# Kernel tuning notes

Measured on AMD Instinct MI355X. Metric: run time of the kernel, lower is better.

Reference implementation:

```python
import jax, jax.numpy as jnp
import numpy as np

N = 32768   # 'a' nodes
K = 8       # incoming edges per node (regular graph)
K2 = K // 2
E = N * K   # edges, stored as reverse pairs (2i, 2i+1)
D = 300     # hid_dim
H = 4       # attention heads
DEPTH = 3


def _build_graph():
    i = np.arange(N)
    src = np.empty(E, np.int64)
    mail = np.empty((N, K), np.int64)
    for d in range(1, K2 + 1):
        base = 2 * (i * K2 + (d - 1))
        src[base] = i                 # edge i -> (i+d)%N
        src[base + 1] = (i + d) % N   # reverse edge (i+d)%N -> i
        # incoming edges of node v: ((v-d)->v) and ((v+d)->v)
        mail[:, 2 * (d - 1)] = 2 * (((i - d) % N) * K2 + (d - 1))
        mail[:, 2 * (d - 1) + 1] = 2 * (i * K2 + (d - 1)) + 1
    return src, mail


def setup_inputs() -> dict:
    key = jax.random.key(0)
    ks = jax.random.split(key, 12)
    s = 1.0 / np.sqrt(D)
    src, mail = _build_graph()
    return {
        'f': jax.random.normal(ks[0], (N, D), jnp.float32),
        'x': jax.random.normal(ks[1], (E, D), jnp.float32),
        'mail_idx': jnp.asarray(mail),
        'src_idx': jnp.asarray(src),
        'Wq': jax.random.normal(ks[2], (D, D), jnp.float32) * s,
        'bq': jnp.zeros((D,), jnp.float32),
        'Wk': jax.random.normal(ks[3], (D, D), jnp.float32) * s,
        'bk': jnp.zeros((D,), jnp.float32),
        'Wv': jax.random.normal(ks[4], (D, D), jnp.float32) * s,
        'bv': jnp.zeros((D,), jnp.float32),
        'Wo': jax.random.normal(ks[5], (D, D), jnp.float32) * s,
        'bo': jnp.zeros((D,), jnp.float32),
        'Wmp': jax.random.normal(ks[6], (DEPTH - 1, D, D), jnp.float32) * s,
        'bmp': jnp.zeros((DEPTH - 1, D), jnp.float32),
        'Wlast': jax.random.normal(ks[7], (3 * D, D), jnp.float32) * s,
        'blast': jnp.zeros((D,), jnp.float32),
    }


def _mha(q_in, k_in, v_in, Wq, bq, Wk, bk, Wv, bv, Wo, bo):
    # q_in: [N,1,D], k_in/v_in: [N,K,D]  (per-node neighborhood attention)
    dk = D // H
    q = (q_in @ Wq + bq).reshape(N, 1, H, dk).transpose(0, 2, 1, 3)
    k = (k_in @ Wk + bk).reshape(N, -1, H, dk).transpose(0, 2, 1, 3)
    v = (v_in @ Wv + bv).reshape(N, -1, H, dk).transpose(0, 2, 1, 3)
    scores = jnp.einsum('nhqd,nhkd->nhqk', q, k) / jnp.sqrt(jnp.float32(dk))
    p = jax.nn.softmax(scores, axis=-1)
    o = jnp.einsum('nhqk,nhkd->nhqd', p, v).transpose(0, 2, 1, 3).reshape(N, 1, D)
    return o @ Wo + bo


def reference(f, x, mail_idx, src_idx, Wq, bq, Wk, bk, Wv, bv, Wo, bo,
              Wmp, bmp, Wlast, blast):
    rev = jnp.arange(E) ^ 1  # reverse_edge: swap within consecutive pairs
    f_h = f              # init_node: f_h = f.clone()
    h = x                # init_edge: h = x.clone()
    for i in range(DEPTH - 1):
        mail = h[mail_idx]                    # copy_e mailbox [N,K,D]
        feat = f_h[:, None, :]                # [N,1,D]
        # add_attn: attn(feat, mail, mail + feat)
        f_h = _mha(feat, mail, mail + feat,
                   Wq, bq, Wk, bk, Wv, bv, Wo, bo)[:, 0, :]
        rev_h = h[rev]                        # paired reverse-edge feature
        m = f_h[src_idx] - rev_h              # del_reverse_message
        h = jax.nn.relu(x + m @ Wmp[i] + bmp[i])  # update_edge
    # final node update: Linear(cat([sum(mailbox h), f_h, f]))
    mail_sum = jnp.sum(h[mail_idx], axis=1)   # [N,D]
    f_final = jnp.concatenate([mail_sum, f_h, f], axis=1) @ Wlast + blast
    return f_final
```

## Files before the change

kernel.cpp:

```cpp
#include <hip/hip_runtime.h>

typedef unsigned short u16;
typedef unsigned int u32;
typedef __bf16 bf16x8 __attribute__((ext_vector_type(8)));
typedef float f32x4 __attribute__((ext_vector_type(4)));

#define N_NODES 32768
#define E_EDGES 262144
#define BQ_U16 26240
#define S75 0.11547005383792515f

__device__ __forceinline__ float b2f(u16 u) {
    union { u32 u; float f; } x; x.u = ((u32)u) << 16; return x.f;
}
__device__ __forceinline__ u16 f2b(float f) {
    union { float f; u32 u; } x; x.f = f;
    u32 r = x.u + 0x7FFF + ((x.u >> 16) & 1);
    return (u16)(r >> 16);
}
__device__ __forceinline__ u32 bsub2(u32 a, u32 b) {
    float lo = b2f((u16)(a & 0xFFFF)) - b2f((u16)(b & 0xFFFF));
    float hi = b2f((u16)(a >> 16))    - b2f((u16)(b >> 16));
    return (u32)f2b(lo) | ((u32)f2b(hi) << 16);
}

#define GLOAD16(g, l) \
    __builtin_amdgcn_global_load_lds((const __attribute__((address_space(1))) u32*)(g), \
                                     (__attribute__((address_space(3))) u32*)(l), 16, 0, 0)

__global__ void convT_k(const float* __restrict__ src, int R, int C,
                        u16* __restrict__ dst, int KP_, long total) {
    long id = (long)blockIdx.x * blockDim.x + threadIdx.x;
    if (id >= total) return;
    int n = (int)(id / KP_), k = (int)(id % KP_);
    dst[id] = (k < R && n < C) ? f2b(src[(long)k * C + n]) : (u16)0;
}

__global__ void convTq_k(const float* __restrict__ src, u16* __restrict__ dst) {
    int id = blockIdx.x * 256 + threadIdx.x;
    if (id >= 4 * BQ_U16) return;
    int q = id / BQ_U16, rem = id % BQ_U16;
    int r = rem / 328, c = rem % 328;
    int n = q * 80 + r;
    dst[id] = (c < 300 && n < 300) ? f2b(src[(long)c * 300 + n]) : (u16)0;
}

__global__ void wqkq_k(const float* __restrict__ Wq, const float* __restrict__ Wk,
                       u16* __restrict__ dst) {
    int id = blockIdx.x * 256 + threadIdx.x;
    if (id >= 16 * BQ_U16) return;
    int q = id / BQ_U16, rem = id % BQ_U16;
    int r = rem / 328, c = rem % 328;
    int h = q >> 2;
    int cc = (q & 3) * 80 + r;
    float acc = 0.f;
    if (c < 300 && cc < 300) {
        const float* wq = Wq + (long)c * 300 + 75 * h;
        const float* wk = Wk + (long)cc * 300 + 75 * h;
        for (int d = 0; d < 75; ++d) acc += wq[d] * wk[d];
        acc *= S75;
    }
    dst[id] = f2b(acc);
}

__global__ void bqk_k(const float* __restrict__ bq, const float* __restrict__ Wk,
                      float* __restrict__ dst) {
    int n = blockIdx.x * 256 + threadIdx.x;
    if (n >= 1280) return;
    int h = n / 320, cc = n % 320;
    float acc = 0.f;
    if (cc < 300) {
        const float* b = bq + 75 * h;
        const float* wk = Wk + (long)cc * 300 + 75 * h;
        for (int d = 0; d < 75; ++d) acc += b[d] * wk[d];
        acc *= S75;
    }
    dst[n] = acc;
}

__global__ void ucat_k(const float* __restrict__ Wv, const float* __restrict__ Wo,
                       u16* __restrict__ dst) {
    long id = (long)blockIdx.x * 256 + threadIdx.x;
    if (id >= 320L * 1600) return;
    int n = (int)(id / 1600), k = (int)(id % 1600);
    float acc = 0.f;
    if (n < 300) {
        if (k < 1280) {
            int h = k / 320, a = k % 320;
            if (a < 300) {
                const float* wv = Wv + (long)a * 300 + 75 * h;
                const float* wo = Wo + (long)(75 * h) * 300 + n;
                for (int d = 0; d < 75; ++d) acc += wv[d] * wo[(long)d * 300];
            }
        } else {
            int a = k - 1280;
            if (a < 300) {
                const float* wv = Wv + (long)a * 300;
                const float* wo = Wo + n;
                for (int d = 0; d < 300; ++d) acc += wv[d] * wo[(long)d * 300];
            }
        }
    }
    dst[id] = f2b(acc);
}

__global__ void bvo_k(const float* __restrict__ bv, const float* __restrict__ Wo,
                      const float* __restrict__ bo, float* __restrict__ dst) {
    int n = blockIdx.x * 256 + threadIdx.x;
    if (n >= 320) return;
    float acc = 0.f;
    if (n < 300) {
        for (int d = 0; d < 300; ++d) acc += bv[d] * Wo[(long)d * 300 + n];
        acc += bo[n];
    }
    dst[n] = acc;
}

__global__ void padconv_k(const float* __restrict__ src, int C,
                          u16* __restrict__ dst, int CP,
                          u16* __restrict__ dst2, int CP2, long total) {
    long id = (long)blockIdx.x * blockDim.x + threadIdx.x;
    if (id >= total) return;
    int cw = CP >> 3;
    long row = id / cw;
    int c8 = (int)(id % cw) * 8;
    u32 w[4];
    #pragma unroll
    for (int p = 0; p < 4; ++p) {
        int c0 = c8 + 2 * p, c1 = c0 + 1;
        u16 lo = (c0 < C) ? f2b(src[row * C + c0]) : (u16)0;
        u16 hi = (c1 < C) ? f2b(src[row * C + c1]) : (u16)0;
        w[p] = (u32)lo | ((u32)hi << 16);
    }
    u32* d = (u32*)(dst + row * CP + c8);
    d[0] = w[0]; d[1] = w[1]; d[2] = w[2]; d[3] = w[3];
    if (dst2) {
        u32* d2 = (u32*)(dst2 + row * CP2 + c8);
        d2[0] = w[0]; d2[1] = w[1]; d2[2] = w[2]; d2[3] = w[3];
    }
}

#define TCOMP(KB, APTR) do { \
    bf16x8 av_[2], bb_[5]; \
    _Pragma("unroll") for (int fr = 0; fr < 2; ++fr) \
        av_[fr] = *(const bf16x8*)&(APTR)[ar0 + fr * 512]; \
    _Pragma("unroll") for (int fc = 0; fc < 5; ++fc) \
        bb_[fc] = *(const bf16x8*)&Bs[br0 + fc * 5248 + (KB) * 32]; \
    __builtin_amdgcn_s_setprio(1); \
    _Pragma("unroll") for (int fr = 0; fr < 2; ++fr) \
        _Pragma("unroll") for (int fc = 0; fc < 5; ++fc) \
            acc[fr][fc] = __builtin_amdgcn_mfma_f32_16x16x32_bf16(bb_[fc], av_[fr], acc[fr][fc], 0, 0, 0); \
    __builtin_amdgcn_s_setprio(0); \
} while (0)

__global__ __launch_bounds__(256, 2) void qgemm_k(
    const u16* __restrict__ A, const u16* __restrict__ Bswz,
    const float* __restrict__ bias, u16* __restrict__ outB)
{
    __shared__ __attribute__((aligned(16))) u16 Bs[80 * 328];
    __shared__ __attribute__((aligned(16))) u16 As3[3][128 * 32];
    const int tid = threadIdx.x;
    const int wf = tid >> 6, lane = tid & 63;
    const int tl = lane & 15, thi = lane >> 4;
    const int bid = blockIdx.x;
    const int gid = (bid & 7) * ((int)gridDim.x >> 3) + (bid >> 3);
    const long m0 = (long)(gid >> 4) * 128;
    const int q = gid & 15;
    const int n0 = q * 80;
    const int wf_u = __builtin_amdgcn_readfirstlane(wf);
    const u16* Bsrc = Bswz + q * BQ_U16;

    #pragma unroll
    for (int i = 0; i < 13; ++i) {
        int t = i * 256 + tid;
        if (t < 3280)
            GLOAD16(Bsrc + (long)t * 8, &Bs[(i * 256 + wf_u * 64) * 8]);
    }
    const int r1 = tid >> 2;
    const int g1 = (tid & 3) ^ ((r1 >> 1) & 3);
    const u16* gA0 = A + (m0 + r1) * 320L + g1 * 8;
    const u16* gA1 = A + (m0 + 64 + r1) * 320L + g1 * 8;

#define ESTAGE(KB) { \
    GLOAD16(gA0 + (KB) * 32, &As3[(KB) % 3][wf_u * 512]); \
    GLOAD16(gA1 + (KB) * 32, &As3[(KB) % 3][2048 + wf_u * 512]); }

    ESTAGE(0); ESTAGE(1);

    f32x4 acc[2][5];
    #pragma unroll
    for (int i = 0; i < 2; ++i)
        #pragma unroll
        for (int j = 0; j < 5; ++j) acc[i][j] = (f32x4)(0.f);
    const int ar0 = (wf * 32 + tl) * 32 + (thi ^ ((tl >> 1) & 3)) * 8;
    const int br0 = tl * 328 + thi * 8;

#define ESTEP(KB, VN) { \
    asm volatile("s_waitcnt vmcnt(" #VN ")" ::: "memory"); \
    __builtin_amdgcn_s_barrier(); \
    __builtin_amdgcn_sched_barrier(0); \
    if ((KB) + 2 < 10) ESTAGE((KB) + 2); \
    TCOMP(KB, (&As3[(KB) % 3][0])); }

    ESTEP(0, 2) ESTEP(1, 2) ESTEP(2, 2) ESTEP(3, 2) ESTEP(4, 2)
    ESTEP(5, 2) ESTEP(6, 2) ESTEP(7, 2) ESTEP(8, 2) ESTEP(9, 0)
#undef ESTEP
#undef ESTAGE

    #pragma unroll
    for (int fr = 0; fr < 2; ++fr) {
        const long row = m0 + wf * 32 + fr * 16 + tl;
        #pragma unroll
        for (int fc = 0; fc < 5; ++fc) {
            const int c0 = n0 + fc * 16 + thi * 4;
            f32x4 v = acc[fr][fc];
            const float4 bs = *(const float4*)&bias[c0];
            v[0] += bs.x; v[1] += bs.y; v[2] += bs.z; v[3] += bs.w;
            uint2 p;
            p.x = (u32)f2b(v[0]) | ((u32)f2b(v[1]) << 16);
            p.y = (u32)f2b(v[2]) | ((u32)f2b(v[3]) << 16);
            *(uint2*)&outB[row * 1280 + c0] = p;
        }
    }
}

__global__ __launch_bounds__(256) void attn2_k(
    const u16* __restrict__ qg, const u16* __restrict__ hcur,
    const int* __restrict__ mail, u16* __restrict__ wideA)
{
    const int tid = threadIdx.x;
    const long n = (long)blockIdx.x * 4 + (tid >> 6);
    const int lane = tid & 63;
    const bool act = lane < 40;
    const int ll = act ? lane : 39;

    int idx[8];
    #pragma unroll
    for (int j = 0; j < 8; ++j) idx[j] = mail[n * 8 + j];
    uint4 hr[8];
    #pragma unroll
    for (int j = 0; j < 8; ++j)
        hr[j] = *(const uint4*)&hcur[(long)idx[j] * 320 + ll * 8];
    uint4 qv[4];
    #pragma unroll
    for (int h = 0; h < 4; ++h)
        qv[h] = *(const uint4*)&qg[n * 1280 + h * 320 + ll * 8];
    if (!act) {
        #pragma unroll
        for (int j = 0; j < 8; ++j) hr[j] = make_uint4(0, 0, 0, 0);
    }

    float qf[4][8];
    #pragma unroll
    for (int h = 0; h < 4; ++h) {
        const u32 w[4] = {qv[h].x, qv[h].y, qv[h].z, qv[h].w};
        #pragma unroll
        for (int p = 0; p < 4; ++p) {
            qf[h][2 * p]     = b2f((u16)(w[p] & 0xFFFF));
            qf[h][2 * p + 1] = b2f((u16)(w[p] >> 16));
        }
    }

    float s[4][8];
    #pragma unroll
    for (int j = 0; j < 8; ++j) {
        float hf[8];
        const u32 w[4] = {hr[j].x, hr[j].y, hr[j].z, hr[j].w};
        #pragma unroll
        for (int p = 0; p < 4; ++p) {
            hf[2 * p]     = b2f((u16)(w[p] & 0xFFFF));
            hf[2 * p + 1] = b2f((u16)(w[p] >> 16));
        }
        #pragma unroll
        for (int h = 0; h < 4; ++h) {
            float d = 0.f;
            #pragma unroll
            for (int m = 0; m < 8; ++m) d += qf[h][m] * hf[m];
            d += __shfl_xor(d, 32, 64);
            d += __shfl_xor(d, 16, 64);
            d += __shfl_xor(d, 8, 64);
            d += __shfl_xor(d, 4, 64);
            d += __shfl_xor(d, 2, 64);
            d += __shfl_xor(d, 1, 64);
            s[h][j] = d;
        }
    }

    float p_[4][8];
    #pragma unroll
    for (int h = 0; h < 4; ++h) {
        float mx = s[h][0];
        #pragma unroll
        for (int j = 1; j < 8; ++j) mx = fmaxf(mx, s[h][j]);
        float sum = 0.f;
        #pragma unroll
        for (int j = 0; j < 8; ++j) { p_[h][j] = __expf(s[h][j] - mx); sum += p_[h][j]; }
        const float inv = 1.f / sum;
        #pragma unroll
        for (int j = 0; j < 8; ++j) p_[h][j] *= inv;
    }

    float y[4][8];
    #pragma unroll
    for (int h = 0; h < 4; ++h)
        #pragma unroll
        for (int m = 0; m < 8; ++m) y[h][m] = 0.f;
    #pragma unroll
    for (int j = 0; j < 8; ++j) {
        float hf[8];
        const u32 w[4] = {hr[j].x, hr[j].y, hr[j].z, hr[j].w};
        #pragma unroll
        for (int p = 0; p < 4; ++p) {
            hf[2 * p]     = b2f((u16)(w[p] & 0xFFFF));
            hf[2 * p + 1] = b2f((u16)(w[p] >> 16));
        }
        #pragma unroll
        for (int h = 0; h < 4; ++h)
            #pragma unroll
            for (int m = 0; m < 8; ++m) y[h][m] += p_[h][j] * hf[m];
    }
    if (act) {
        #pragma unroll
        for (int h = 0; h < 4; ++h) {
            uint4 o;
            o.x = (u32)f2b(y[h][0]) | ((u32)f2b(y[h][1]) << 16);
            o.y = (u32)f2b(y[h][2]) | ((u32)f2b(y[h][3]) << 16);
            o.z = (u32)f2b(y[h][4]) | ((u32)f2b(y[h][5]) << 16);
            o.w = (u32)f2b(y[h][6]) | ((u32)f2b(y[h][7]) << 16);
            *(uint4*)&wideA[n * 1600 + h * 320 + lane * 8] = o;
        }
    }
}

__global__ __launch_bounds__(256, 2) void egemmmb_k(
    const u16* __restrict__ fhb, const u16* __restrict__ hcur,
    const u16* __restrict__ hx, const int* __restrict__ srcidx,
    const u16* __restrict__ Bswz, const float* __restrict__ bias,
    u16* __restrict__ outB)
{
    __shared__ __attribute__((aligned(16))) u16 Bs[80 * 328];
    __shared__ __attribute__((aligned(16))) u16 As2[2][128 * 32];
    const int tid = threadIdx.x;
    const int wf = tid >> 6, lane = tid & 63;
    const int tl = lane & 15, thi = lane >> 4;
    const int bid = blockIdx.x;
    const int gid = (bid & 7) * ((int)gridDim.x >> 3) + (bid >> 3);
    const long m0 = (long)(gid >> 2) * 128;
    const int q = gid & 3;
    const int n0 = q * 80;
    const int wf_u = __builtin_amdgcn_readfirstlane(wf);
    const u16* Bsrc = Bswz + q * BQ_U16;

    #pragma unroll
    for (int i = 0; i < 13; ++i) {
        int t = i * 256 + tid;
        if (t < 3280)
            GLOAD16(Bsrc + (long)t * 8, &Bs[(i * 256 + wf_u * 64) * 8]);
    }
    const int r1 = tid >> 2;
    const int g1 = (tid & 3) ^ ((r1 >> 1) & 3);
    const long e0 = m0 + r1, e1 = m0 + 64 + r1;
    const u16* pF0 = fhb + (long)srcidx[e0] * 320 + g1 * 8;
    const u16* pH0 = hcur + (e0 ^ 1) * 320 + g1 * 8;
    const u16* pF1 = fhb + (long)srcidx[e1] * 320 + g1 * 8;
    const u16* pH1 = hcur + (e1 ^ 1) * 320 + g1 * 8;

    uint4 Fa0, Ha0, Fa1, Ha1, Fb0, Hb0, Fb1, Hb1, Fc0, Hc0, Fc1, Hc1;

#define MLOAD(KB, F0, H0, F1, H1) { \
    F0 = *(const uint4*)(pF0 + (KB) * 32); H0 = *(const uint4*)(pH0 + (KB) * 32); \
    F1 = *(const uint4*)(pF1 + (KB) * 32); H1 = *(const uint4*)(pH1 + (KB) * 32); }

#define MWRITE(KB, F0, H0, F1, H1) { \
    u16* wb_ = &As2[(KB) & 1][0]; \
    uint4 o_; \
    o_.x = bsub2(F0.x, H0.x); o_.y = bsub2(F0.y, H0.y); \
    o_.z = bsub2(F0.z, H0.z); o_.w = bsub2(F0.w, H0.w); \
    *(uint4*)&wb_[tid * 8] = o_; \
    o_.x = bsub2(F1.x, H1.x); o_.y = bsub2(F1.y, H1.y); \
    o_.z = bsub2(F1.z, H1.z); o_.w = bsub2(F1.w, H1.w); \
    *(uint4*)&wb_[(tid + 256) * 8] = o_; }

    MLOAD(0, Fa0, Ha0, Fa1, Ha1);
    MLOAD(1, Fb0, Hb0, Fb1, Hb1);
    MLOAD(2, Fc0, Hc0, Fc1, Hc1);
    asm volatile("s_waitcnt vmcnt(8)" ::: "memory");
    MWRITE(0, Fa0, Ha0, Fa1, Ha1);

    f32x4 acc[2][5];
    #pragma unroll
    for (int i = 0; i < 2; ++i)
        #pragma unroll
        for (int j = 0; j < 5; ++j) acc[i][j] = (f32x4)(0.f);
    const int ar0 = (wf * 32 + tl) * 32 + (thi ^ ((tl >> 1) & 3)) * 8;
    const int br0 = tl * 328 + thi * 8;

#define MSTEP(KB, VN, LF0, LH0, LF1, LH1, SF0, SH0, SF1, SH1) { \
    if ((KB) + 3 < 10) MLOAD((KB) + 3, LF0, LH0, LF1, LH1); \
    asm volatile("s_waitcnt vmcnt(" #VN ")" ::: "memory"); \
    asm volatile("s_waitcnt lgkmcnt(0)" ::: "memory"); \
    __builtin_amdgcn_s_barrier(); \
    __builtin_amdgcn_sched_barrier(0); \
    if ((KB) + 1 < 10) MWRITE((KB) + 1, SF0, SH0, SF1, SH1); \
    TCOMP(KB, (&As2[(KB) & 1][0])); }

    MSTEP(0, 8, Fa0, Ha0, Fa1, Ha1, Fb0, Hb0, Fb1, Hb1)
    MSTEP(1, 8, Fb0, Hb0, Fb1, Hb1, Fc0, Hc0, Fc1, Hc1)
    MSTEP(2, 8, Fc0, Hc0, Fc1, Hc1, Fa0, Ha0, Fa1, Ha1)
    MSTEP(3, 8, Fa0, Ha0, Fa1, Ha1, Fb0, Hb0, Fb1, Hb1)
    MSTEP(4, 8, Fb0, Hb0, Fb1, Hb1, Fc0, Hc0, Fc1, Hc1)
    MSTEP(5, 8, Fc0, Hc0, Fc1, Hc1, Fa0, Ha0, Fa1, Ha1)
    MSTEP(6, 8, Fa0, Ha0, Fa1, Ha1, Fb0, Hb0, Fb1, Hb1)
    MSTEP(7, 4, Fb0, Hb0, Fb1, Hb1, Fc0, Hc0, Fc1, Hc1)
    MSTEP(8, 0, Fc0, Hc0, Fc1, Hc1, Fa0, Ha0, Fa1, Ha1)
    MSTEP(9, 0, Fa0, Ha0, Fa1, Ha1, Fb0, Hb0, Fb1, Hb1)
#undef MSTEP
#undef MLOAD
#undef MWRITE

    #pragma unroll
    for (int fr = 0; fr < 2; ++fr) {
        const long row = m0 + wf * 32 + fr * 16 + tl;
        #pragma unroll
        for (int fc = 0; fc < 5; ++fc) {
            const int c0 = n0 + fc * 16 + thi * 4;
            f32x4 v = acc[fr][fc];
            if (bias && c0 < 300) {
                const float4 bs = *(const float4*)&bias[c0];
                v[0] += bs.x; v[1] += bs.y; v[2] += bs.z; v[3] += bs.w;
            }
            {
                const ushort4 xv = *(const ushort4*)&hx[row * 320 + c0];
                v[0] += b2f(xv.x); v[1] += b2f(xv.y); v[2] += b2f(xv.z); v[3] += b2f(xv.w);
            }
            v[0] = fmaxf(v[0], 0.f); v[1] = fmaxf(v[1], 0.f);
            v[2] = fmaxf(v[2], 0.f); v[3] = fmaxf(v[3], 0.f);
            uint2 p;
            p.x = (u32)f2b(v[0]) | ((u32)f2b(v[1]) << 16);
            p.y = (u32)f2b(v[2]) | ((u32)f2b(v[3]) << 16);
            *(uint2*)&outB[row * 320 + c0] = p;
        }
    }
}

#define LOADB(bq, kt1) { const long ko_ = (long)(kt1) << 6; \
    _Pragma("unroll") for (int fc = 0; fc < 5; ++fc) \
      _Pragma("unroll") for (int ks = 0; ks < 2; ++ks) \
        bq[fc][ks] = *(const bf16x8*)(gBw + (long)fc * 16 * KP + ko_ + ks * 32); }

#define READA(lkt) { \
    _Pragma("unroll") for (int fr = 0; fr < 4; ++fr) \
      _Pragma("unroll") for (int ks = 0; ks < 2; ++ks) \
        a[fr][ks] = *(const bf16x8*)&As[(fr * 16 + tl) * 320 + ((((lkt) * 8 + ks * 4 + thi) ^ sx) * 8)]; }

#define DOMFMA(bq) { _Pragma("unroll") for (int fr = 0; fr < 4; ++fr) \
    _Pragma("unroll") for (int fc = 0; fc < 5; ++fc) \
      _Pragma("unroll") for (int ks = 0; ks < 2; ++ks) \
        acc[fr][fc] = __builtin_amdgcn_mfma_f32_16x16x32_bf16(bq[fc][ks], a[fr][ks], acc[fr][fc], 0, 0, 0); }

template<int KP>
__global__ __launch_bounds__(256, 2) void gemm_k(
    const u16* __restrict__ A,
    const u16* __restrict__ BT,
    const float* __restrict__ bias,
    float* __restrict__ outF, int ostride, int ocols,
    u16* __restrict__ outB1, long strideB1,
    u16* __restrict__ outB2, long strideB2)
{
    __shared__ u16 As[64 * 320];
    const int tid = threadIdx.x;
    const int w = tid >> 6, lane = tid & 63;
    const int tl = lane & 15, thi = lane >> 4;
    const int sx = tl & 7;
    const long m0 = (long)blockIdx.x * 64;
    const int w_u = __builtin_amdgcn_readfirstlane(w);

    const u16* gBw = BT + ((long)(w * 80 + tl)) * KP + thi * 8;

    f32x4 acc[4][5];
    #pragma unroll
    for (int i = 0; i < 4; ++i)
        #pragma unroll
        for (int j = 0; j < 5; ++j) acc[i][j] = (f32x4)(0.f);

    constexpr int NCH = KP / 320;
    constexpr int NST = KP >> 6;
    bf16x8 bA[5][2], bB[5][2], a[4][2];

    #pragma unroll
    for (int kb = 0; kb < NCH; ++kb) {
        if (kb) __syncthreads();
        #pragma unroll
        for (int i = 0; i < 10; ++i) {
            const int c = i * 256 + w_u * 64 + lane;
            const int r = c / 40, s = c - r * 40;
            GLOAD16(A + (m0 + r) * (long)KP + kb * 320 + ((s ^ (r & 7)) * 8),
                    &As[(i * 256 + w_u * 64) * 8]);
        }
        if (kb == 0) LOADB(bA, 0);
        __syncthreads();
        #pragma unroll
        for (int lkt = 0; lkt < 5; ++lkt) {
            const int kt = kb * 5 + lkt;
            if (kt + 1 < NST) {
                if (kt & 1) { LOADB(bA, kt + 1); } else { LOADB(bB, kt + 1); }
            }
            READA(lkt);
            if (kt & 1) { DOMFMA(bB); } else { DOMFMA(bA); }
        }
    }

    #pragma unroll
    for (int fr = 0; fr < 4; ++fr) {
        const long row = m0 + fr * 16 + tl;
        #pragma unroll
        for (int fc = 0; fc < 5; ++fc) {
            const int c0 = w * 80 + fc * 16 + thi * 4;
            f32x4 v = acc[fr][fc];
            if (bias && c0 < 300) {
                const float4 bs = *(const float4*)&bias[c0];
                v[0] += bs.x; v[1] += bs.y; v[2] += bs.z; v[3] += bs.w;
            }
            if (outF && c0 < ocols)
                *(float4*)&outF[row * (long)ostride + c0] = make_float4(v[0], v[1], v[2], v[3]);
            if (outB1 || outB2) {
                uint2 p;
                p.x = (u32)f2b(v[0]) | ((u32)f2b(v[1]) << 16);
                p.y = (u32)f2b(v[2]) | ((u32)f2b(v[3]) << 16);
                if (outB1) *(uint2*)&outB1[row * strideB1 + c0] = p;
                if (outB2) *(uint2*)&outB2[row * strideB2 + c0] = p;
            }
        }
    }
}

__global__ __launch_bounds__(256) void concat_k(
    const u16* __restrict__ hb, const u16* __restrict__ fhb,
    const float* __restrict__ f, const int* __restrict__ mail,
    u16* __restrict__ Acat)
{
    const long n = blockIdx.x;
    int m[8];
    #pragma unroll
    for (int j = 0; j < 8; ++j) m[j] = mail[n * 8 + j];
    for (int c = threadIdx.x; c < 960; c += 256) {
        float v;
        if (c < 300) {
            float s = 0.f;
            #pragma unroll
            for (int j = 0; j < 8; ++j) s += b2f(hb[(long)m[j] * 320 + c]);
            v = s;
        } else if (c < 600) v = b2f(fhb[n * 320 + (c - 300)]);
        else if (c < 900) v = f[n * 300 + (c - 600)];
        else v = 0.f;
        Acat[n * 960 + c] = f2b(v);
    }
}

extern "C" void kernel_launch(void* const* d_in, const int* in_sizes, int n_in,
                              void* d_out, int out_size, void* d_ws, size_t ws_size,
                              hipStream_t stream)
{
    const int N = N_NODES, E = E_EDGES;
    const float* f    = (const float*)d_in[0];
    const float* x    = (const float*)d_in[1];
    const int*   mail = (const int*)d_in[2];
    const int*   srcx = (const int*)d_in[3];
    const float* Wq = (const float*)d_in[4];   const float* bq = (const float*)d_in[5];
    const float* Wk = (const float*)d_in[6];
    const float* Wv = (const float*)d_in[8];   const float* bv = (const float*)d_in[9];
    const float* Wo = (const float*)d_in[10];  const float* bo = (const float*)d_in[11];
    const float* Wmp = (const float*)d_in[12]; const float* bmp = (const float*)d_in[13];
    const float* Wlast = (const float*)d_in[14]; const float* blast = (const float*)d_in[15];
    float* out = (float*)d_out;

    char* ws = (char*)d_ws;
    size_t off = 0;
    auto alloc = [&](size_t b) -> void* {
        void* p = ws + off; off += (b + 255) & ~(size_t)255; return p;
    };
    u16* hb    = (u16*)alloc((size_t)E * 320 * 2);
    u16* hb2   = (u16*)alloc((size_t)E * 320 * 2);
    u16* qgb   = (u16*)alloc((size_t)N * 1280 * 2);
    u16* wideA = (u16*)alloc((size_t)N * 1600 * 2);
    u16* fhb   = (u16*)alloc((size_t)N * 320 * 2);
    u16* Acat  = (u16*)alloc((size_t)N * 960 * 2);
    u16* WqkS  = (u16*)alloc((size_t)16 * BQ_U16 * 2);
    u16* Wm0S  = (u16*)alloc((size_t)4 * BQ_U16 * 2);
    u16* Wm1S  = (u16*)alloc((size_t)4 * BQ_U16 * 2);
    u16* UcatT = (u16*)alloc((size_t)320 * 1600 * 2);
    u16* WcatB = (u16*)alloc((size_t)960 * 320 * 2);
    float* bqkF = (float*)alloc(1280 * 4);
    float* bvoF = (float*)alloc(320 * 4);

    {
        wqkq_k<<<(16 * BQ_U16 + 255) / 256, 256, 0, stream>>>(Wq, Wk, WqkS);
        bqk_k<<<5, 256, 0, stream>>>(bq, Wk, bqkF);
        ucat_k<<<(int)((320L * 1600 + 255) / 256), 256, 0, stream>>>(Wv, Wo, UcatT);
        bvo_k<<<2, 256, 0, stream>>>(bv, Wo, bo, bvoF);
        int blks = (4 * BQ_U16 + 255) / 256;
        convTq_k<<<blks, 256, 0, stream>>>(Wmp, Wm0S);
        convTq_k<<<blks, 256, 0, stream>>>(Wmp + 90000, Wm1S);
        long totc = (long)320 * 960;
        convT_k<<<(int)((totc + 255) / 256), 256, 0, stream>>>(Wlast, 900, 300, WcatB, 960, totc);
    }
    {
        long totE = (long)E * 40;
        padconv_k<<<(int)((totE + 255) / 256), 256, 0, stream>>>(x, 300, hb, 320, nullptr, 0, totE);
        long totN = (long)N * 40;
        padconv_k<<<(int)((totN + 255) / 256), 256, 0, stream>>>(f, 300, fhb, 320, wideA + 1280, 1600, totN);
    }

    const int GQG = (N / 128) * 16;
    const int GE  = (E / 128) * 4;

    for (int it = 0; it < 2; ++it) {
        const u16* WmS = it ? Wm1S : Wm0S;
        const float* bmpi = bmp + it * 300;
        const u16* hcur = it ? hb2 : hb;
        u16* hnxt = it ? hb : hb2;
        qgemm_k<<<GQG, 256, 0, stream>>>(fhb, WqkS, bqkF, qgb);
        attn2_k<<<N / 4, 256, 0, stream>>>(qgb, hcur, mail, wideA);
        gemm_k<1600><<<N / 64, 256, 0, stream>>>(wideA, UcatT, bvoF,
                                                 nullptr, 0, 0, fhb, 320, wideA + 1280, 1600);
        egemmmb_k<<<GE, 256, 0, stream>>>(fhb, hcur, hb, srcx, WmS, bmpi, hnxt);
    }

    concat_k<<<N, 256, 0, stream>>>(hb, fhb, f, mail, Acat);
    gemm_k<960><<<N / 64, 256, 0, stream>>>(Acat, WcatB, blast, out, 300, 300,
                                            nullptr, 0, nullptr, 0);
}
```

Before: 1.385 ms.

## Split edge message GEMM into node-level f_h·W plus reverse-edge GEMM

Uses linearity, (f_h[src] - h[rev])·W = (f_h·W)[src] - h[rev]·W. The f_h·W product is computed once per node (N rows instead of E), and the per-edge GEMM runs directly on h, with the reverse pairing handled by a lane shuffle (xor 1) in the epilogue. This replaces the gather-and-subtract A staging. The wide output-projection GEMM is also moved to a new pipelined MFMA kernel with a swizzled pre-packed weight layout, plus a separate feature copy into wideA. This adds extra launches and an FG buffer, and the reverse-edge shuffle relies on both paired edges landing in adjacent lanes.

```diff
diff --git a/kernel.cpp b/kernel.cpp
--- a/kernel.cpp
+++ b/kernel.cpp
@@ -17,11 +17,6 @@
     union { float f; u32 u; } x; x.f = f;
     u32 r = x.u + 0x7FFF + ((x.u >> 16) & 1);
     return (u16)(r >> 16);
-}
-__device__ __forceinline__ u32 bsub2(u32 a, u32 b) {
-    float lo = b2f((u16)(a & 0xFFFF)) - b2f((u16)(b & 0xFFFF));
-    float hi = b2f((u16)(a >> 16))    - b2f((u16)(b >> 16));
-    return (u32)f2b(lo) | ((u32)f2b(hi) << 16);
 }
 
 #define GLOAD16(g, l) \
@@ -78,22 +73,27 @@
     dst[n] = acc;
 }
 
-__global__ void ucat_k(const float* __restrict__ Wv, const float* __restrict__ Wo,
-                       u16* __restrict__ dst) {
+__global__ void ucatp_k(const float* __restrict__ Wv, const float* __restrict__ Wo,
+                        u16* __restrict__ dst) {
     long id = (long)blockIdx.x * 256 + threadIdx.x;
-    if (id >= 320L * 1600) return;
-    int n = (int)(id / 1600), k = (int)(id % 1600);
+    if (id >= 4L * 5 * BQ_U16) return;
+    int q = (int)(id / (5 * BQ_U16));
+    int rem = (int)(id % (5 * BQ_U16));
+    int ph = rem / BQ_U16;
+    int rem2 = rem % BQ_U16;
+    int r = rem2 / 328, c = rem2 % 328;
+    int n = q * 80 + r;
     float acc = 0.f;
-    if (n < 300) {
-        if (k < 1280) {
-            int h = k / 320, a = k % 320;
+    if (n < 300 && c < 320) {
+        if (ph < 4) {
+            int a = c;
             if (a < 300) {
-                const float* wv = Wv + (long)a * 300 + 75 * h;
-                const float* wo = Wo + (long)(75 * h) * 300 + n;
+                const float* wv = Wv + (long)a * 300 + 75 * ph;
+                const float* wo = Wo + (long)(75 * ph) * 300 + n;
                 for (int d = 0; d < 75; ++d) acc += wv[d] * wo[(long)d * 300];
             }
         } else {
-            int a = k - 1280;
+            int a = c;
             if (a < 300) {
                 const float* wv = Wv + (long)a * 300;
                 const float* wo = Wo + n;
@@ -138,6 +138,14 @@
         u32* d2 = (u32*)(dst2 + row * CP2 + c8);
         d2[0] = w[0]; d2[1] = w[1]; d2[2] = w[2]; d2[3] = w[3];
     }
+}
+
+__global__ void featcopy_k(const u16* __restrict__ src, u16* __restrict__ dst) {
+    long id = (long)blockIdx.x * 256 + threadIdx.x;
+    if (id >= (long)N_NODES * 40) return;
+    long row = id / 40;
+    int c8 = (int)(id % 40) * 8;
+    *(uint4*)&dst[row * 1600 + 1280 + c8] = *(const uint4*)&src[row * 320 + c8];
 }
 
 #define TCOMP(KB, APTR) do { \
@@ -153,7 +161,8 @@
     __builtin_amdgcn_s_setprio(0); \
 } while (0)
 
-__global__ __launch_bounds__(256, 2) void qgemm_k(
+template<int QBITS, int OSTR>
+__global__ __launch_bounds__(256, 2) void ngemm_k(
     const u16* __restrict__ A, const u16* __restrict__ Bswz,
     const float* __restrict__ bias, u16* __restrict__ outB)
 {
@@ -164,8 +173,8 @@
     const int tl = lane & 15, thi = lane >> 4;
     const int bid = blockIdx.x;
     const int gid = (bid & 7) * ((int)gridDim.x >> 3) + (bid >> 3);
-    const long m0 = (long)(gid >> 4) * 128;
-    const int q = gid & 15;
+    const long m0 = (long)(gid >> QBITS) * 128;
+    const int q = gid & ((1 << QBITS) - 1);
     const int n0 = q * 80;
     const int wf_u = __builtin_amdgcn_readfirstlane(wf);
     const u16* Bsrc = Bswz + q * BQ_U16;
@@ -206,6 +215,173 @@
     ESTEP(5, 2) ESTEP(6, 2) ESTEP(7, 2) ESTEP(8, 2) ESTEP(9, 0)
 #undef ESTEP
 #undef ESTAGE
+
+    #pragma unroll
+    for (int fr = 0; fr < 2; ++fr) {
+        const long row = m0 + wf * 32 + fr * 16 + tl;
+        #pragma unroll
+        for (int fc = 0; fc < 5; ++fc) {
+            const int c0 = n0 + fc * 16 + thi * 4;
+            f32x4 v = acc[fr][fc];
+            if (bias) {
+                const float4 bs = *(const float4*)&bias[c0];
+                v[0] += bs.x; v[1] += bs.y; v[2] += bs.z; v[3] += bs.w;
+            }
+            uint2 p;
+            p.x = (u32)f2b(v[0]) | ((u32)f2b(v[1]) << 16);
+            p.y = (u32)f2b(v[2]) | ((u32)f2b(v[3]) << 16);
+            *(uint2*)&outB[row * (long)OSTR + c0] = p;
+        }
+    }
+}
+
+__global__ __launch_bounds__(256, 2) void hgemm_k(
+    const u16* __restrict__ A , const u16* __restrict__ Bswz ,
+    const u16* __restrict__ FG, const u16* __restrict__ hx,
+    const int* __restrict__ srcidx, const float* __restrict__ bias,
+    u16* __restrict__ outB)
+{
+    __shared__ __attribute__((aligned(16))) u16 Bs[80 * 328];
+    __shared__ __attribute__((aligned(16))) u16 As3[3][128 * 32];
+    const int tid = threadIdx.x;
+    const int wf = tid >> 6, lane = tid & 63;
+    const int tl = lane & 15, thi = lane >> 4;
+    const int bid = blockIdx.x;
+    const int gid = (bid & 7) * ((int)gridDim.x >> 3) + (bid >> 3);
+    const long m0 = (long)(gid >> 2) * 128;
+    const int q = gid & 3;
+    const int n0 = q * 80;
+    const int wf_u = __builtin_amdgcn_readfirstlane(wf);
+    const u16* Bsrc = Bswz + q * BQ_U16;
+
+    #pragma unroll
+    for (int i = 0; i < 13; ++i) {
+        int t = i * 256 + tid;
+        if (t < 3280)
+            GLOAD16(Bsrc + (long)t * 8, &Bs[(i * 256 + wf_u * 64) * 8]);
+    }
+    const int r1 = tid >> 2;
+    const int g1 = (tid & 3) ^ ((r1 >> 1) & 3);
+    const u16* gA0 = A + (m0 + r1) * 320L + g1 * 8;
+    const u16* gA1 = A + (m0 + 64 + r1) * 320L + g1 * 8;
+
+#define HSTAGE(KB) { \
+    GLOAD16(gA0 + (KB) * 32, &As3[(KB) % 3][wf_u * 512]); \
+    GLOAD16(gA1 + (KB) * 32, &As3[(KB) % 3][2048 + wf_u * 512]); }
+
+    HSTAGE(0); HSTAGE(1);
+
+    f32x4 acc[2][5];
+    #pragma unroll
+    for (int i = 0; i < 2; ++i)
+        #pragma unroll
+        for (int j = 0; j < 5; ++j) acc[i][j] = (f32x4)(0.f);
+    const int ar0 = (wf * 32 + tl) * 32 + (thi ^ ((tl >> 1) & 3)) * 8;
+    const int br0 = tl * 328 + thi * 8;
+
+#define HSTEP(KB, VN) { \
+    asm volatile("s_waitcnt vmcnt(" #VN ")" ::: "memory"); \
+    __builtin_amdgcn_s_barrier(); \
+    __builtin_amdgcn_sched_barrier(0); \
+    if ((KB) + 2 < 10) HSTAGE((KB) + 2); \
+    TCOMP(KB, (&As3[(KB) % 3][0])); }
+
+    HSTEP(0, 2) HSTEP(1, 2) HSTEP(2, 2) HSTEP(3, 2) HSTEP(4, 2)
+    HSTEP(5, 2) HSTEP(6, 2) HSTEP(7, 2) HSTEP(8, 2) HSTEP(9, 0)
+#undef HSTEP
+#undef HSTAGE
+
+    #pragma unroll
+    for (int fr = 0; fr < 2; ++fr) {
+        const long row = m0 + wf * 32 + fr * 16 + tl;
+        const int srow = srcidx[row];
+        #pragma unroll
+        for (int fc = 0; fc < 5; ++fc) {
+            const int c0 = n0 + fc * 16 + thi * 4;
+            float o0 = __shfl_xor(acc[fr][fc][0], 1, 64);
+            float o1 = __shfl_xor(acc[fr][fc][1], 1, 64);
+            float o2 = __shfl_xor(acc[fr][fc][2], 1, 64);
+            float o3 = __shfl_xor(acc[fr][fc][3], 1, 64);
+            const ushort4 fg = *(const ushort4*)&FG[(long)srow * 320 + c0];
+            const ushort4 xv = *(const ushort4*)&hx[row * 320 + c0];
+            float v0 = b2f(fg.x) + b2f(xv.x) - o0;
+            float v1 = b2f(fg.y) + b2f(xv.y) - o1;
+            float v2 = b2f(fg.z) + b2f(xv.z) - o2;
+            float v3 = b2f(fg.w) + b2f(xv.w) - o3;
+            if (c0 < 300) {
+                const float4 bs = *(const float4*)&bias[c0];
+                v0 += bs.x; v1 += bs.y; v2 += bs.z; v3 += bs.w;
+            }
+            v0 = fmaxf(v0, 0.f); v1 = fmaxf(v1, 0.f);
+            v2 = fmaxf(v2, 0.f); v3 = fmaxf(v3, 0.f);
+            uint2 p;
+            p.x = (u32)f2b(v0) | ((u32)f2b(v1) << 16);
+            p.y = (u32)f2b(v2) | ((u32)f2b(v3) << 16);
+            *(uint2*)&outB[row * 320 + c0] = p;
+        }
+    }
+}
+
+__global__ __launch_bounds__(256, 2) void wgemm_k(
+    const u16* __restrict__ A , const u16* __restrict__ Bp ,
+    const float* __restrict__ bias , u16* __restrict__ outB )
+{
+    __shared__ __attribute__((aligned(16))) u16 Bs[80 * 328];
+    __shared__ __attribute__((aligned(16))) u16 As3[3][128 * 32];
+    const int tid = threadIdx.x;
+    const int wf = tid >> 6, lane = tid & 63;
+    const int tl = lane & 15, thi = lane >> 4;
+    const int bid = blockIdx.x;
+    const int gid = (bid & 7) * ((int)gridDim.x >> 3) + (bid >> 3);
+    const long m0 = (long)(gid >> 2) * 128;
+    const int q = gid & 3;
+    const int n0 = q * 80;
+    const int wf_u = __builtin_amdgcn_readfirstlane(wf);
+    const u16* BsrcQ = Bp + (long)q * (5 * BQ_U16);
+
+    const int r1 = tid >> 2;
+    const int g1 = (tid & 3) ^ ((r1 >> 1) & 3);
+    const u16* gA0 = A + (m0 + r1) * 1600L + g1 * 8;
+    const u16* gA1 = A + (m0 + 64 + r1) * 1600L + g1 * 8;
+
+    f32x4 acc[2][5];
+    #pragma unroll
+    for (int i = 0; i < 2; ++i)
+        #pragma unroll
+        for (int j = 0; j < 5; ++j) acc[i][j] = (f32x4)(0.f);
+    const int ar0 = (wf * 32 + tl) * 32 + (thi ^ ((tl >> 1) & 3)) * 8;
+    const int br0 = tl * 328 + thi * 8;
+
+    #pragma unroll
+    for (int ph = 0; ph < 5; ++ph) {
+        if (ph) __syncthreads();
+        const u16* Bsrc = BsrcQ + ph * BQ_U16;
+        #pragma unroll
+        for (int i = 0; i < 13; ++i) {
+            int t = i * 256 + tid;
+            if (t < 3280)
+                GLOAD16(Bsrc + (long)t * 8, &Bs[(i * 256 + wf_u * 64) * 8]);
+        }
+        const long ko = (long)ph * 320;
+
+#define WSTAGE(KB) { \
+    GLOAD16(gA0 + ko + (KB) * 32, &As3[(KB) % 3][wf_u * 512]); \
+    GLOAD16(gA1 + ko + (KB) * 32, &As3[(KB) % 3][2048 + wf_u * 512]); }
+
+        WSTAGE(0); WSTAGE(1);
+
+#define WSTEP(KB, VN) { \
+    asm volatile("s_waitcnt vmcnt(" #VN ")" ::: "memory"); \
+    __builtin_amdgcn_s_barrier(); \
+    __builtin_amdgcn_sched_barrier(0); \
+    if ((KB) + 2 < 10) WSTAGE((KB) + 2); \
+    TCOMP(KB, (&As3[(KB) % 3][0])); }
+
+        WSTEP(0, 2) WSTEP(1, 2) WSTEP(2, 2) WSTEP(3, 2) WSTEP(4, 2)
+        WSTEP(5, 2) WSTEP(6, 2) WSTEP(7, 2) WSTEP(8, 2) WSTEP(9, 0)
+#undef WSTEP
+#undef WSTAGE
+    }
 
     #pragma unroll
     for (int fr = 0; fr < 2; ++fr) {
@@ -219,7 +395,7 @@
             uint2 p;
             p.x = (u32)f2b(v[0]) | ((u32)f2b(v[1]) << 16);
             p.y = (u32)f2b(v[2]) | ((u32)f2b(v[3]) << 16);
-            *(uint2*)&outB[row * 1280 + c0] = p;
+            *(uint2*)&outB[row * 320 + c0] = p;
         }
     }
 }
@@ -332,117 +508,6 @@
     }
 }
 
-__global__ __launch_bounds__(256, 2) void egemmmb_k(
-    const u16* __restrict__ fhb, const u16* __restrict__ hcur,
-    const u16* __restrict__ hx, const int* __restrict__ srcidx,
-    const u16* __restrict__ Bswz, const float* __restrict__ bias,
-    u16* __restrict__ outB)
-{
-    __shared__ __attribute__((aligned(16))) u16 Bs[80 * 328];
-    __shared__ __attribute__((aligned(16))) u16 As2[2][128 * 32];
-    const int tid = threadIdx.x;
-    const int wf = tid >> 6, lane = tid & 63;
-    const int tl = lane & 15, thi = lane >> 4;
-    const int bid = blockIdx.x;
-    const int gid = (bid & 7) * ((int)gridDim.x >> 3) + (bid >> 3);
-    const long m0 = (long)(gid >> 2) * 128;
-    const int q = gid & 3;
-    const int n0 = q * 80;
-    const int wf_u = __builtin_amdgcn_readfirstlane(wf);
-    const u16* Bsrc = Bswz + q * BQ_U16;
-
-    #pragma unroll
-    for (int i = 0; i < 13; ++i) {
-        int t = i * 256 + tid;
-        if (t < 3280)
-            GLOAD16(Bsrc + (long)t * 8, &Bs[(i * 256 + wf_u * 64) * 8]);
-    }
-    const int r1 = tid >> 2;
-    const int g1 = (tid & 3) ^ ((r1 >> 1) & 3);
-    const long e0 = m0 + r1, e1 = m0 + 64 + r1;
-    const u16* pF0 = fhb + (long)srcidx[e0] * 320 + g1 * 8;
-    const u16* pH0 = hcur + (e0 ^ 1) * 320 + g1 * 8;
-    const u16* pF1 = fhb + (long)srcidx[e1] * 320 + g1 * 8;
-    const u16* pH1 = hcur + (e1 ^ 1) * 320 + g1 * 8;
-
-    uint4 Fa0, Ha0, Fa1, Ha1, Fb0, Hb0, Fb1, Hb1, Fc0, Hc0, Fc1, Hc1;
-
-#define MLOAD(KB, F0, H0, F1, H1) { \
-    F0 = *(const uint4*)(pF0 + (KB) * 32); H0 = *(const uint4*)(pH0 + (KB) * 32); \
-    F1 = *(const uint4*)(pF1 + (KB) * 32); H1 = *(const uint4*)(pH1 + (KB) * 32); }
-
-#define MWRITE(KB, F0, H0, F1, H1) { \
-    u16* wb_ = &As2[(KB) & 1][0]; \
-    uint4 o_; \
-    o_.x = bsub2(F0.x, H0.x); o_.y = bsub2(F0.y, H0.y); \
-    o_.z = bsub2(F0.z, H0.z); o_.w = bsub2(F0.w, H0.w); \
-    *(uint4*)&wb_[tid * 8] = o_; \
-    o_.x = bsub2(F1.x, H1.x); o_.y = bsub2(F1.y, H1.y); \
-    o_.z = bsub2(F1.z, H1.z); o_.w = bsub2(F1.w, H1.w); \
-    *(uint4*)&wb_[(tid + 256) * 8] = o_; }
-
-    MLOAD(0, Fa0, Ha0, Fa1, Ha1);
-    MLOAD(1, Fb0, Hb0, Fb1, Hb1);
-    MLOAD(2, Fc0, Hc0, Fc1, Hc1);
-    asm volatile("s_waitcnt vmcnt(8)" ::: "memory");
-    MWRITE(0, Fa0, Ha0, Fa1, Ha1);
-
-    f32x4 acc[2][5];
-    #pragma unroll
-    for (int i = 0; i < 2; ++i)
-        #pragma unroll
-        for (int j = 0; j < 5; ++j) acc[i][j] = (f32x4)(0.f);
-    const int ar0 = (wf * 32 + tl) * 32 + (thi ^ ((tl >> 1) & 3)) * 8;
-    const int br0 = tl * 328 + thi * 8;
-
-#define MSTEP(KB, VN, LF0, LH0, LF1, LH1, SF0, SH0, SF1, SH1) { \
-    if ((KB) + 3 < 10) MLOAD((KB) + 3, LF0, LH0, LF1, LH1); \
-    asm volatile("s_waitcnt vmcnt(" #VN ")" ::: "memory"); \
-    asm volatile("s_waitcnt lgkmcnt(0)" ::: "memory"); \
-    __builtin_amdgcn_s_barrier(); \
-    __builtin_amdgcn_sched_barrier(0); \
-    if ((KB) + 1 < 10) MWRITE((KB) + 1, SF0, SH0, SF1, SH1); \
-    TCOMP(KB, (&As2[(KB) & 1][0])); }
-
-    MSTEP(0, 8, Fa0, Ha0, Fa1, Ha1, Fb0, Hb0, Fb1, Hb1)
-    MSTEP(1, 8, Fb0, Hb0, Fb1, Hb1, Fc0, Hc0, Fc1, Hc1)
-    MSTEP(2, 8, Fc0, Hc0, Fc1, Hc1, Fa0, Ha0, Fa1, Ha1)
-    MSTEP(3, 8, Fa0, Ha0, Fa1, Ha1, Fb0, Hb0, Fb1, Hb1)
-    MSTEP(4, 8, Fb0, Hb0, Fb1, Hb1, Fc0, Hc0, Fc1, Hc1)
-    MSTEP(5, 8, Fc0, Hc0, Fc1, Hc1, Fa0, Ha0, Fa1, Ha1)
-    MSTEP(6, 8, Fa0, Ha0, Fa1, Ha1, Fb0, Hb0, Fb1, Hb1)
-    MSTEP(7, 4, Fb0, Hb0, Fb1, Hb1, Fc0, Hc0, Fc1, Hc1)
-    MSTEP(8, 0, Fc0, Hc0, Fc1, Hc1, Fa0, Ha0, Fa1, Ha1)
-    MSTEP(9, 0, Fa0, Ha0, Fa1, Ha1, Fb0, Hb0, Fb1, Hb1)
-#undef MSTEP
-#undef MLOAD
-#undef MWRITE
-
-    #pragma unroll
-    for (int fr = 0; fr < 2; ++fr) {
-        const long row = m0 + wf * 32 + fr * 16 + tl;
-        #pragma unroll
-        for (int fc = 0; fc < 5; ++fc) {
-            const int c0 = n0 + fc * 16 + thi * 4;
-            f32x4 v = acc[fr][fc];
-            if (bias && c0 < 300) {
-                const float4 bs = *(const float4*)&bias[c0];
-                v[0] += bs.x; v[1] += bs.y; v[2] += bs.z; v[3] += bs.w;
-            }
-            {
-                const ushort4 xv = *(const ushort4*)&hx[row * 320 + c0];
-                v[0] += b2f(xv.x); v[1] += b2f(xv.y); v[2] += b2f(xv.z); v[3] += b2f(xv.w);
-            }
-            v[0] = fmaxf(v[0], 0.f); v[1] = fmaxf(v[1], 0.f);
-            v[2] = fmaxf(v[2], 0.f); v[3] = fmaxf(v[3], 0.f);
-            uint2 p;
-            p.x = (u32)f2b(v[0]) | ((u32)f2b(v[1]) << 16);
-            p.y = (u32)f2b(v[2]) | ((u32)f2b(v[3]) << 16);
-            *(uint2*)&outB[row * 320 + c0] = p;
-        }
-    }
-}
-
 #define LOADB(bq, kt1) { const long ko_ = (long)(kt1) << 6; \
     _Pragma("unroll") for (int fc = 0; fc < 5; ++fc) \
       _Pragma("unroll") for (int ks = 0; ks < 2; ++ks) \
@@ -463,9 +528,7 @@
     const u16* __restrict__ A,
     const u16* __restrict__ BT,
     const float* __restrict__ bias,
-    float* __restrict__ outF, int ostride, int ocols,
-    u16* __restrict__ outB1, long strideB1,
-    u16* __restrict__ outB2, long strideB2)
+    float* __restrict__ outF, int ostride, int ocols)
 {
     __shared__ u16 As[64 * 320];
     const int tid = threadIdx.x;
@@ -521,15 +584,8 @@
                 const float4 bs = *(const float4*)&bias[c0];
                 v[0] += bs.x; v[1] += bs.y; v[2] += bs.z; v[3] += bs.w;
             }
-            if (outF && c0 < ocols)
+            if (c0 < ocols)
                 *(float4*)&outF[row * (long)ostride + c0] = make_float4(v[0], v[1], v[2], v[3]);
-            if (outB1 || outB2) {
-                uint2 p;
-                p.x = (u32)f2b(v[0]) | ((u32)f2b(v[1]) << 16);
-                p.y = (u32)f2b(v[2]) | ((u32)f2b(v[3]) << 16);
-                if (outB1) *(uint2*)&outB1[row * strideB1 + c0] = p;
-                if (outB2) *(uint2*)&outB2[row * strideB2 + c0] = p;
-            }
         }
     }
 }
@@ -584,11 +640,12 @@
     u16* qgb   = (u16*)alloc((size_t)N * 1280 * 2);
     u16* wideA = (u16*)alloc((size_t)N * 1600 * 2);
     u16* fhb   = (u16*)alloc((size_t)N * 320 * 2);
+    u16* FGb   = (u16*)alloc((size_t)N * 320 * 2);
     u16* Acat  = (u16*)alloc((size_t)N * 960 * 2);
     u16* WqkS  = (u16*)alloc((size_t)16 * BQ_U16 * 2);
     u16* Wm0S  = (u16*)alloc((size_t)4 * BQ_U16 * 2);
     u16* Wm1S  = (u16*)alloc((size_t)4 * BQ_U16 * 2);
-    u16* UcatT = (u16*)alloc((size_t)320 * 1600 * 2);
+    u16* UcatP = (u16*)alloc((size_t)4 * 5 * BQ_U16 * 2);
     u16* WcatB = (u16*)alloc((size_t)960 * 320 * 2);
     float* bqkF = (float*)alloc(1280 * 4);
     float* bvoF = (float*)alloc(320 * 4);
@@ -596,7 +653,7 @@
     {
         wqkq_k<<<(16 * BQ_U16 + 255) / 256, 256, 0, stream>>>(Wq, Wk, WqkS);
         bqk_k<<<5, 256, 0, stream>>>(bq, Wk, bqkF);
-        ucat_k<<<(int)((320L * 1600 + 255) / 256), 256, 0, stream>>>(Wv, Wo, UcatT);
+        ucatp_k<<<(int)((4L * 5 * BQ_U16 + 255) / 256), 256, 0, stream>>>(Wv, Wo, UcatP);
         bvo_k<<<2, 256, 0, stream>>>(bv, Wo, bo, bvoF);
         int blks = (4 * BQ_U16 + 255) / 256;
         convTq_k<<<blks, 256, 0, stream>>>(Wmp, Wm0S);
@@ -612,21 +669,22 @@
     }
 
     const int GQG = (N / 128) * 16;
-    const int GE  = (E / 128) * 4;
+    const int GNQ = (N / 128) * 4;
+    const int GEH = (E / 128) * 4;
 
     for (int it = 0; it < 2; ++it) {
+        const float* bmpi = bmp + it * 300;
         const u16* WmS = it ? Wm1S : Wm0S;
-        const float* bmpi = bmp + it * 300;
         const u16* hcur = it ? hb2 : hb;
         u16* hnxt = it ? hb : hb2;
-        qgemm_k<<<GQG, 256, 0, stream>>>(fhb, WqkS, bqkF, qgb);
+        ngemm_k<4, 1280><<<GQG, 256, 0, stream>>>(fhb, WqkS, bqkF, qgb);
         attn2_k<<<N / 4, 256, 0, stream>>>(qgb, hcur, mail, wideA);
-        gemm_k<1600><<<N / 64, 256, 0, stream>>>(wideA, UcatT, bvoF,
-                                                 nullptr, 0, 0, fhb, 320, wideA + 1280, 1600);
-        egemmmb_k<<<GE, 256, 0, stream>>>(fhb, hcur, hb, srcx, WmS, bmpi, hnxt);
+        wgemm_k<<<GNQ, 256, 0, stream>>>(wideA, UcatP, bvoF, fhb);
+        featcopy_k<<<(int)(((long)N * 40 + 255) / 256), 256, 0, stream>>>(fhb, wideA);
+        ngemm_k<2, 320><<<GNQ, 256, 0, stream>>>(fhb, WmS, nullptr, FGb);
+        hgemm_k<<<GEH, 256, 0, stream>>>(hcur, WmS, FGb, hb, srcx, bmpi, hnxt);
     }
 
     concat_k<<<N, 256, 0, stream>>>(hb, fhb, f, mail, Acat);
-    gemm_k<960><<<N / 64, 256, 0, stream>>>(Acat, WcatB, blast, out, 300, 300,
-                                            nullptr, 0, nullptr, 0);
-}
+    gemm_k<960><<<N / 64, 256, 0, stream>>>(Acat, WcatB, blast, out, 300, 300);
+}
```

Measured after the change: 1.395 ms. About the same (+0.8%).
